# Performance work log

Hardware: AMD Instinct MI355X
Metric: run time of the kernel (lower is better)

## Reference

```python
import jax, jax.numpy as jnp
import numpy as np

EPS = 1e-5

def _instance_norm(x):
    # PyG InstanceNorm with batch=None, affine=False: per-channel normalize
    # over the node/edge dimension with biased variance.
    mean = jnp.mean(x, axis=0, keepdims=True)
    var = jnp.mean(jnp.square(x - mean), axis=0, keepdims=True)
    return (x - mean) * jax.lax.rsqrt(var + EPS)

def setup_inputs() -> dict:
    key = jax.random.key(0)
    ks = jax.random.split(key, 8)
    N, E, H = 50000, 800000, 64
    s1 = 1.0 / np.sqrt(2 * H)
    s2 = 1.0 / np.sqrt(4 * H)
    s3 = 1.0 / np.sqrt(H)
    return {
        "emb": jax.random.normal(ks[0], (N, H), dtype=jnp.float32),
        "edge_index": jax.random.randint(ks[1], (2, E), 0, N, dtype=jnp.int64),
        "W1": jax.random.normal(ks[2], (2 * H, 4 * H), dtype=jnp.float32) * s1,
        "b1": jnp.zeros((4 * H,), dtype=jnp.float32),
        "W2": jax.random.normal(ks[3], (4 * H, H), dtype=jnp.float32) * s2,
        "b2": jnp.zeros((H,), dtype=jnp.float32),
        "W3": jax.random.normal(ks[4], (H, 1), dtype=jnp.float32) * s3,
        "b3": jnp.zeros((1,), dtype=jnp.float32),
    }

def reference(emb, edge_index, W1, b1, W2, b2, W3, b3):
    # Dropout is identity in eval mode.
    col, row = edge_index[0], edge_index[1]
    f12 = jnp.concatenate([emb[col], emb[row]], axis=-1)  # [E, 2H]
    h = jax.nn.relu(_instance_norm(f12 @ W1 + b1))        # [E, 4H]
    h = jax.nn.relu(_instance_norm(h @ W2 + b2))          # [E, H]
    return h @ W3 + b3                                    # [E, 1]
```

## Files before the change

### kernel.cpp

```cpp
#include <hip/hip_runtime.h>
#include <stdint.h>

#define EPS 1e-5f

typedef __attribute__((ext_vector_type(8))) short bf16x8;
typedef __attribute__((ext_vector_type(4))) float f32x4;

__device__ __forceinline__ short f2bf(float f) {
  union { float f; unsigned u; } c; c.f = f;
  unsigned r = (c.u + 0x7FFFu + ((c.u >> 16) & 1u)) >> 16;
  return (short)r;
}
__device__ __forceinline__ float bf2f(unsigned short s) {
  union { unsigned u; float f; } c; c.u = ((unsigned)s) << 16;
  return c.f;
}

#define WS_SUM1 0
#define WS_SQ1  256
#define WS_SUM2 512
#define WS_SQ2  576
#define WS_M1   640
#define WS_I1   896
#define WS_M2   1152
#define WS_I2   1216
#define H2S_BYTE_OFF 8192

__global__ void k_zero(float* ws) {
  for (int i = threadIdx.x; i < 640; i += 256) ws[i] = 0.f;
}

__global__ void k_finalize(float* ws, int n, int so, int qo, int mo, int io, float invE) {
  int j = threadIdx.x;
  if (j < n) {
    float m = ws[so + j] * invE;
    float var = ws[qo + j] * invE - m * m;
    ws[mo + j] = m;
    ws[io + j] = rsqrtf(var + EPS);
  }
}

template <int MODE>
__global__ __launch_bounds__(256, 2) void fused_pass(
    const float* __restrict__ emb, const int* __restrict__ ei,
    const float* __restrict__ W1, const float* __restrict__ b1,
    const float* __restrict__ W2, const float* __restrict__ b2,
    const float* __restrict__ W3, const float* __restrict__ b3,
    float* __restrict__ ws, unsigned short* __restrict__ h2s,
    float* __restrict__ out, int E, int storeH2) {
  extern __shared__ __align__(16) char lds[];
  const int tid = threadIdx.x;
  const int lane = tid & 63;
  const int w = tid >> 6;
  const int l15 = lane & 15;
  const int l4 = lane >> 4;

  bf16x8 B1[4][4];
#pragma unroll
  for (int ni = 0; ni < 4; ++ni)
#pragma unroll
    for (int kk = 0; kk < 4; ++kk) {
      const int c = w * 64 + ni * 16 + l15;
      const int kb = kk * 32 + l4 * 8;
      bf16x8 v;
#pragma unroll
      for (int i = 0; i < 8; ++i) v[i] = f2bf(W1[(kb + i) * 256 + c]);
      B1[ni][kk] = v;
    }
  float b1v[4], m1v[4] = {0, 0, 0, 0}, i1v[4] = {0, 0, 0, 0};
#pragma unroll
  for (int ni = 0; ni < 4; ++ni) {
    const int c = w * 64 + ni * 16 + l15;
    b1v[ni] = b1[c];
    if (MODE >= 1) { m1v[ni] = ws[WS_M1 + c]; i1v[ni] = ws[WS_I1 + c]; }
  }
  bf16x8 B2[8];
  float b2v = 0.f, m2v = 0.f, i2v = 0.f, w3v = 0.f;
  if (MODE >= 1) {
#pragma unroll
    for (int kk = 0; kk < 8; ++kk) {
      const int c = w * 16 + l15;
      const int kb = kk * 32 + l4 * 8;
      bf16x8 v;
#pragma unroll
      for (int i = 0; i < 8; ++i) v[i] = f2bf(W2[(kb + i) * 64 + c]);
      B2[kk] = v;
    }
    b2v = b2[w * 16 + l15];
    if (MODE == 2) {
      m2v = ws[WS_M2 + w * 16 + l15];
      i2v = ws[WS_I2 + w * 16 + l15];
      w3v = W3[w * 16 + l15];
    }
  }

  float sAcc[4] = {0, 0, 0, 0}, qAcc[4] = {0, 0, 0, 0};
  float s2A = 0.f, q2A = 0.f;

  const int nTiles = E >> 6;
  for (int t = blockIdx.x; t < nTiles; t += gridDim.x) {
    const int e0 = t << 6;
    __syncthreads();

    {
      const int e = tid >> 2, q = tid & 3;
      const int nidx = (q < 2) ? ei[e0 + e] : ei[E + e0 + e];
      const float* src = emb + (long)nidx * 64 + (q & 1) * 32;
#pragma unroll
      for (int jj = 0; jj < 4; ++jj) {
        float4 fa = *reinterpret_cast<const float4*>(src + jj * 8);
        float4 fb = *reinterpret_cast<const float4*>(src + jj * 8 + 4);
        bf16x8 p;
        p[0] = f2bf(fa.x); p[1] = f2bf(fa.y); p[2] = f2bf(fa.z); p[3] = f2bf(fa.w);
        p[4] = f2bf(fb.x); p[5] = f2bf(fb.y); p[6] = f2bf(fb.z); p[7] = f2bf(fb.w);
        int byte = e * 256 + q * 64 + jj * 16;
        byte ^= (e & 7) << 4;
        *reinterpret_cast<bf16x8*>(lds + byte) = p;
      }
      if (MODE == 2) {
        if (tid < 64) reinterpret_cast<float*>(lds + 49152)[tid] = 0.f;
      }
    }
    __syncthreads();

    f32x4 acc[4][4];
#pragma unroll
    for (int mi = 0; mi < 4; ++mi)
#pragma unroll
      for (int ni = 0; ni < 4; ++ni) acc[mi][ni] = f32x4{0.f, 0.f, 0.f, 0.f};
#pragma unroll
    for (int kk = 0; kk < 4; ++kk) {
      bf16x8 af[4];
#pragma unroll
      for (int mi = 0; mi < 4; ++mi) {
        const int row = mi * 16 + l15;
        int byte = row * 256 + kk * 64 + l4 * 16;
        byte ^= (row & 7) << 4;
        af[mi] = *reinterpret_cast<const bf16x8*>(lds + byte);
      }
#pragma unroll
      for (int ni = 0; ni < 4; ++ni)
#pragma unroll
        for (int mi = 0; mi < 4; ++mi)
          acc[mi][ni] = __builtin_amdgcn_mfma_f32_16x16x32_bf16(af[mi], B1[ni][kk], acc[mi][ni], 0, 0, 0);
    }

    if (MODE == 0) {
#pragma unroll
      for (int mi = 0; mi < 4; ++mi)
#pragma unroll
        for (int ni = 0; ni < 4; ++ni)
#pragma unroll
          for (int r = 0; r < 4; ++r) {
            const float v = acc[mi][ni][r] + b1v[ni];
            sAcc[ni] += v;
            qAcc[ni] += v * v;
          }
    } else {
      char* g = lds + 16384;
#pragma unroll
      for (int mi = 0; mi < 4; ++mi)
#pragma unroll
        for (int ni = 0; ni < 4; ++ni) {
          const int c = w * 64 + ni * 16 + l15;
#pragma unroll
          for (int r = 0; r < 4; ++r) {
            const int row = mi * 16 + l4 * 4 + r;
            float v = (acc[mi][ni][r] + b1v[ni] - m1v[ni]) * i1v[ni];
            v = v > 0.f ? v : 0.f;
            int byte = row * 512 + c * 2;
            byte ^= (row & 7) << 4;
            *reinterpret_cast<short*>(g + byte) = f2bf(v);
          }
        }
      __syncthreads();

      f32x4 acc2[4];
#pragma unroll
      for (int mi = 0; mi < 4; ++mi) acc2[mi] = f32x4{0.f, 0.f, 0.f, 0.f};
#pragma unroll
      for (int kk = 0; kk < 8; ++kk) {
#pragma unroll
        for (int mi = 0; mi < 4; ++mi) {
          const int row = mi * 16 + l15;
          int byte = row * 512 + kk * 64 + l4 * 16;
          byte ^= (row & 7) << 4;
          const bf16x8 a2 = *reinterpret_cast<const bf16x8*>(g + byte);
          acc2[mi] = __builtin_amdgcn_mfma_f32_16x16x32_bf16(a2, B2[kk], acc2[mi], 0, 0, 0);
        }
      }

      if (MODE == 1) {
#pragma unroll
        for (int mi = 0; mi < 4; ++mi)
#pragma unroll
          for (int r = 0; r < 4; ++r) {
            const float v = acc2[mi][r] + b2v;
            s2A += v;
            q2A += v * v;
            if (storeH2) {
              const int row = e0 + mi * 16 + l4 * 4 + r;
              h2s[(size_t)row * 64 + w * 16 + l15] = (unsigned short)f2bf(v);
            }
          }
      } else {
        float* outp = reinterpret_cast<float*>(lds + 49152);
#pragma unroll
        for (int mi = 0; mi < 4; ++mi)
#pragma unroll
          for (int r = 0; r < 4; ++r) {
            const float v = acc2[mi][r] + b2v;
            float z = (v - m2v) * i2v;
            z = z > 0.f ? z : 0.f;
            float pv = z * w3v;
            pv += __shfl_xor(pv, 1);
            pv += __shfl_xor(pv, 2);
            pv += __shfl_xor(pv, 4);
            pv += __shfl_xor(pv, 8);
            if (l15 == 0) atomicAdd(&outp[mi * 16 + l4 * 4 + r], pv);
          }
        __syncthreads();
        if (tid < 64) out[e0 + tid] = outp[tid] + b3[0];
      }
    }
  }

  if (MODE == 0) {
#pragma unroll
    for (int ni = 0; ni < 4; ++ni) {
      float s = sAcc[ni], q = qAcc[ni];
      s += __shfl_xor(s, 16); s += __shfl_xor(s, 32);
      q += __shfl_xor(q, 16); q += __shfl_xor(q, 32);
      if (lane < 16) {
        atomicAdd(&ws[WS_SUM1 + w * 64 + ni * 16 + lane], s);
        atomicAdd(&ws[WS_SQ1 + w * 64 + ni * 16 + lane], q);
      }
    }
  }
  if (MODE == 1) {
    float s = s2A, q = q2A;
    s += __shfl_xor(s, 16); s += __shfl_xor(s, 32);
    q += __shfl_xor(q, 16); q += __shfl_xor(q, 32);
    if (lane < 16) {
      atomicAdd(&ws[WS_SUM2 + w * 16 + lane], s);
      atomicAdd(&ws[WS_SQ2 + w * 16 + lane], q);
    }
  }
}

__global__ void k_out(const unsigned short* __restrict__ h2s, const float* __restrict__ ws,
                      const float* __restrict__ W3, const float* __restrict__ b3,
                      float* __restrict__ out, int E) {
  __shared__ float sm[64], si[64], sw[64];
  const int tid = threadIdx.x;
  if (tid < 64) {
    sm[tid] = ws[WS_M2 + tid];
    si[tid] = ws[WS_I2 + tid];
    sw[tid] = W3[tid];
  }
  __syncthreads();
  const int e = blockIdx.x * 256 + tid;
  if (e >= E) return;
  const unsigned short* rp = h2s + (size_t)e * 64;
  float a = 0.f;
#pragma unroll
  for (int jj = 0; jj < 8; ++jj) {
    const bf16x8 v8 = *reinterpret_cast<const bf16x8*>(rp + jj * 8);
#pragma unroll
    for (int i = 0; i < 8; ++i) {
      const int j = jj * 8 + i;
      const float v = bf2f((unsigned short)v8[i]);
      float z = (v - sm[j]) * si[j];
      z = z > 0.f ? z : 0.f;
      a += z * sw[j];
    }
  }
  out[e] = a + b3[0];
}

extern "C" void kernel_launch(void* const* d_in, const int* in_sizes, int n_in,
                              void* d_out, int out_size, void* d_ws, size_t ws_size,
                              hipStream_t stream) {
  (void)n_in; (void)out_size;
  const float* emb = (const float*)d_in[0];
  const int* ei = (const int*)d_in[1];
  const float* W1 = (const float*)d_in[2];
  const float* b1 = (const float*)d_in[3];
  const float* W2 = (const float*)d_in[4];
  const float* b2 = (const float*)d_in[5];
  const float* W3 = (const float*)d_in[6];
  const float* b3 = (const float*)d_in[7];
  float* out = (float*)d_out;
  float* ws = (float*)d_ws;
  unsigned short* h2s = (unsigned short*)((char*)d_ws + H2S_BYTE_OFF);

  const int E = in_sizes[1] / 2;
  const int storeH2 = (ws_size >= (size_t)H2S_BYTE_OFF + (size_t)E * 64 * 2) ? 1 : 0;
  const float invE = 1.0f / (float)E;

  k_zero<<<1, 256, 0, stream>>>(ws);
  fused_pass<0><<<768, 256, 16384, stream>>>(emb, ei, W1, b1, W2, b2, W3, b3, ws, h2s, out, E, storeH2);
  k_finalize<<<1, 256, 0, stream>>>(ws, 256, WS_SUM1, WS_SQ1, WS_M1, WS_I1, invE);
  fused_pass<1><<<512, 256, 49152, stream>>>(emb, ei, W1, b1, W2, b2, W3, b3, ws, h2s, out, E, storeH2);
  k_finalize<<<1, 256, 0, stream>>>(ws, 64, WS_SUM2, WS_SQ2, WS_M2, WS_I2, invE);
  if (storeH2) {
    k_out<<<(E + 255) / 256, 256, 0, stream>>>(h2s, ws, W3, b3, out, E);
  } else {
    fused_pass<2><<<512, 256, 49152 + 256, stream>>>(emb, ei, W1, b1, W2, b2, W3, b3, ws, h2s, out, E, storeH2);
  }
}
```

Baseline: 845.4 us.

## Cache gathered bf16 edge features in workspace and reuse via async LDS loads

Pass 0 now writes the gathered, bf16-converted and swizzled [E,128] edge feature tiles to a workspace buffer, and pass 1 loads them straight into LDS with global_load_lds instead of redoing the random emb gather and conversion. The layer-2 staging buffer now reuses the same LDS region, with an extra barrier, which halves LDS per block. Launch bounds go to 4 blocks per CU and grids to 1024. The cost is an extra ~200MB of workspace writes and reads in exchange for avoiding a second random gather, and the path only runs if the workspace is large enough.

```diff
diff --git a/kernel.cpp b/kernel.cpp
--- a/kernel.cpp
+++ b/kernel.cpp
@@ -15,6 +15,11 @@
   union { unsigned u; float f; } c; c.u = ((unsigned)s) << 16;
   return c.f;
 }
+
+#define ASYNC_COPY16(gsrc, ldst)                                                   \
+  __builtin_amdgcn_global_load_lds(                                                \
+      (const __attribute__((address_space(1))) void*)(gsrc),                       \
+      (__attribute__((address_space(3))) void*)(ldst), 16, 0, 0)
 
 #define WS_SUM1 0
 #define WS_SQ1  256
@@ -40,14 +45,14 @@
   }
 }
 
-template <int MODE>
-__global__ __launch_bounds__(256, 2) void fused_pass(
+template <int MODE, int XT>
+__global__ __launch_bounds__(256, 4) void fused_pass(
     const float* __restrict__ emb, const int* __restrict__ ei,
     const float* __restrict__ W1, const float* __restrict__ b1,
     const float* __restrict__ W2, const float* __restrict__ b2,
     const float* __restrict__ W3, const float* __restrict__ b3,
     float* __restrict__ ws, unsigned short* __restrict__ h2s,
-    float* __restrict__ out, int E, int storeH2) {
+    char* __restrict__ f12s, float* __restrict__ out, int E, int storeH2) {
   extern __shared__ __align__(16) char lds[];
   const int tid = threadIdx.x;
   const int lane = tid & 63;
@@ -102,7 +107,13 @@
     const int e0 = t << 6;
     __syncthreads();
 
-    {
+    if (MODE == 1 && XT == 1) {
+      const char* src = f12s + (size_t)t * 16384 + w * 4096 + lane * 16;
+      char* dst = lds + w * 4096;
+#pragma unroll
+      for (int r = 0; r < 4; ++r)
+        ASYNC_COPY16(src + r * 1024, dst + r * 1024);
+    } else {
       const int e = tid >> 2, q = tid & 3;
       const int nidx = (q < 2) ? ei[e0 + e] : ei[E + e0 + e];
       const float* src = emb + (long)nidx * 64 + (q & 1) * 32;
@@ -117,11 +128,21 @@
         byte ^= (e & 7) << 4;
         *reinterpret_cast<bf16x8*>(lds + byte) = p;
       }
-      if (MODE == 2) {
-        if (tid < 64) reinterpret_cast<float*>(lds + 49152)[tid] = 0.f;
-      }
+    }
+    if (MODE == 2) {
+      if (tid < 64) reinterpret_cast<float*>(lds + 32768)[tid] = 0.f;
     }
     __syncthreads();
+
+    if (MODE == 0 && XT == 1) {
+      const char* srcL = lds + w * 4096;
+      char* dstG = f12s + (size_t)t * 16384 + w * 4096;
+#pragma unroll
+      for (int r = 0; r < 4; ++r) {
+        const bf16x8 v = *reinterpret_cast<const bf16x8*>(srcL + r * 1024 + lane * 16);
+        *reinterpret_cast<bf16x8*>(dstG + r * 1024 + lane * 16) = v;
+      }
+    }
 
     f32x4 acc[4][4];
 #pragma unroll
@@ -157,7 +178,9 @@
             qAcc[ni] += v * v;
           }
     } else {
-      char* g = lds + 16384;
+      __syncthreads();
+
+      char* g = lds;
 #pragma unroll
       for (int mi = 0; mi < 4; ++mi)
 #pragma unroll
@@ -204,7 +227,7 @@
             }
           }
       } else {
-        float* outp = reinterpret_cast<float*>(lds + 49152);
+        float* outp = reinterpret_cast<float*>(lds + 32768);
 #pragma unroll
         for (int mi = 0; mi < 4; ++mi)
 #pragma unroll
@@ -295,17 +318,26 @@
   unsigned short* h2s = (unsigned short*)((char*)d_ws + H2S_BYTE_OFF);
 
   const int E = in_sizes[1] / 2;
-  const int storeH2 = (ws_size >= (size_t)H2S_BYTE_OFF + (size_t)E * 64 * 2) ? 1 : 0;
+  const size_t h2bytes = (size_t)E * 64 * 2;
+  const size_t f12bytes = (size_t)E * 128 * 2;
+  char* f12s = (char*)d_ws + H2S_BYTE_OFF + h2bytes;
+  const int storeH2 = (ws_size >= (size_t)H2S_BYTE_OFF + h2bytes) ? 1 : 0;
+  const int storeF12 = (ws_size >= (size_t)H2S_BYTE_OFF + h2bytes + f12bytes) ? 1 : 0;
   const float invE = 1.0f / (float)E;
 
   k_zero<<<1, 256, 0, stream>>>(ws);
-  fused_pass<0><<<768, 256, 16384, stream>>>(emb, ei, W1, b1, W2, b2, W3, b3, ws, h2s, out, E, storeH2);
+  if (storeF12)
+    fused_pass<0, 1><<<1024, 256, 16384, stream>>>(emb, ei, W1, b1, W2, b2, W3, b3, ws, h2s, f12s, out, E, storeH2);
+  else
+    fused_pass<0, 0><<<1024, 256, 16384, stream>>>(emb, ei, W1, b1, W2, b2, W3, b3, ws, h2s, f12s, out, E, storeH2);
   k_finalize<<<1, 256, 0, stream>>>(ws, 256, WS_SUM1, WS_SQ1, WS_M1, WS_I1, invE);
-  fused_pass<1><<<512, 256, 49152, stream>>>(emb, ei, W1, b1, W2, b2, W3, b3, ws, h2s, out, E, storeH2);
+  if (storeF12)
+    fused_pass<1, 1><<<1024, 256, 32768, stream>>>(emb, ei, W1, b1, W2, b2, W3, b3, ws, h2s, f12s, out, E, storeH2);
+  else
+    fused_pass<1, 0><<<1024, 256, 32768, stream>>>(emb, ei, W1, b1, W2, b2, W3, b3, ws, h2s, f12s, out, E, storeH2);
   k_finalize<<<1, 256, 0, stream>>>(ws, 64, WS_SUM2, WS_SQ2, WS_M2, WS_I2, invE);
-  if (storeH2) {
+  if (storeH2)
     k_out<<<(E + 255) / 256, 256, 0, stream>>>(h2s, ws, W3, b3, out, E);
-  } else {
-    fused_pass<2><<<512, 256, 49152 + 256, stream>>>(emb, ei, W1, b1, W2, b2, W3, b3, ws, h2s, out, E, storeH2);
-  }
-}
+  else
+    fused_pass<2, 0><<<1024, 256, 33024, stream>>>(emb, ei, W1, b1, W2, b2, W3, b3, ws, h2s, f12s, out, E, storeH2);
+}
```

Measured after the change: 1.198 ms. 1.42x slower.

## Materialize bf16 layer-1 activations to avoid recomputing gather and first GEMM

Applied to the files above, without the earlier changes.

Adds a pass that gathers embeddings, computes the first GEMM once, accumulates its column statistics and writes the bf16 pre-norm activations to workspace as a swizzled LDS image. A second pass streams that image back with async global-to-LDS copies, applies norm and ReLU, and runs the second GEMM. This replaces the old scheme that recomputed the gather and first GEMM in the second pass. The cost is about 400MB of extra HBM traffic, and the path only runs when the workspace is large enough.

```diff
diff --git a/kernel.cpp b/kernel.cpp
--- a/kernel.cpp
+++ b/kernel.cpp
@@ -15,6 +15,11 @@
   union { unsigned u; float f; } c; c.u = ((unsigned)s) << 16;
   return c.f;
 }
+
+#define ASYNC_COPY16(gsrc, ldst)                                                   \
+  __builtin_amdgcn_global_load_lds(                                                \
+      (const __attribute__((address_space(1))) void*)(gsrc),                       \
+      (__attribute__((address_space(3))) void*)(ldst), 16, 0, 0)
 
 #define WS_SUM1 0
 #define WS_SQ1  256
@@ -37,6 +42,245 @@
     float var = ws[qo + j] * invE - m * m;
     ws[mo + j] = m;
     ws[io + j] = rsqrtf(var + EPS);
+  }
+}
+
+__global__ __launch_bounds__(256, 2) void k_pass_a(
+    const float* __restrict__ emb, const int* __restrict__ ei,
+    const float* __restrict__ W1, const float* __restrict__ b1,
+    float* __restrict__ ws, char* __restrict__ h1img, int E) {
+  extern __shared__ __align__(16) char lds[];
+  const int tid = threadIdx.x;
+  const int lane = tid & 63;
+  const int w = tid >> 6;
+  const int l15 = lane & 15;
+  const int l4 = lane >> 4;
+
+  bf16x8 B1[4][4];
+#pragma unroll
+  for (int ni = 0; ni < 4; ++ni)
+#pragma unroll
+    for (int kk = 0; kk < 4; ++kk) {
+      const int c = w * 64 + ni * 16 + l15;
+      const int kb = kk * 32 + l4 * 8;
+      bf16x8 v;
+#pragma unroll
+      for (int i = 0; i < 8; ++i) v[i] = f2bf(W1[(kb + i) * 256 + c]);
+      B1[ni][kk] = v;
+    }
+  float b1v[4];
+#pragma unroll
+  for (int ni = 0; ni < 4; ++ni) b1v[ni] = b1[w * 64 + ni * 16 + l15];
+
+  float sAcc[4] = {0, 0, 0, 0}, qAcc[4] = {0, 0, 0, 0};
+
+  const int nTiles = E >> 6;
+  const int e_ = tid >> 2, q_ = tid & 3;
+
+  float4 pf[8];
+  {
+    const int e0 = blockIdx.x << 6;
+    const int nidx = (q_ < 2) ? ei[e0 + e_] : ei[E + e0 + e_];
+    const float* src = emb + (long)nidx * 64 + (q_ & 1) * 32;
+#pragma unroll
+    for (int jj = 0; jj < 8; ++jj)
+      pf[jj] = *reinterpret_cast<const float4*>(src + jj * 4);
+  }
+
+  for (int t = blockIdx.x; t < nTiles; t += gridDim.x) {
+#pragma unroll
+    for (int jj = 0; jj < 4; ++jj) {
+      bf16x8 p;
+      p[0] = f2bf(pf[2 * jj].x); p[1] = f2bf(pf[2 * jj].y);
+      p[2] = f2bf(pf[2 * jj].z); p[3] = f2bf(pf[2 * jj].w);
+      p[4] = f2bf(pf[2 * jj + 1].x); p[5] = f2bf(pf[2 * jj + 1].y);
+      p[6] = f2bf(pf[2 * jj + 1].z); p[7] = f2bf(pf[2 * jj + 1].w);
+      int byte = e_ * 256 + q_ * 64 + jj * 16;
+      byte ^= (e_ & 7) << 4;
+      *reinterpret_cast<bf16x8*>(lds + byte) = p;
+    }
+    __syncthreads();
+
+    {
+      const int tn = t + (int)gridDim.x;
+      const int tv = (tn < nTiles) ? tn : t;
+      const int e0n = tv << 6;
+      const int nidx = (q_ < 2) ? ei[e0n + e_] : ei[E + e0n + e_];
+      const float* src = emb + (long)nidx * 64 + (q_ & 1) * 32;
+#pragma unroll
+      for (int jj = 0; jj < 8; ++jj)
+        pf[jj] = *reinterpret_cast<const float4*>(src + jj * 4);
+    }
+
+    f32x4 acc[4][4];
+#pragma unroll
+    for (int mi = 0; mi < 4; ++mi)
+#pragma unroll
+      for (int ni = 0; ni < 4; ++ni) acc[mi][ni] = f32x4{0.f, 0.f, 0.f, 0.f};
+#pragma unroll
+    for (int kk = 0; kk < 4; ++kk) {
+      bf16x8 af[4];
+#pragma unroll
+      for (int mi = 0; mi < 4; ++mi) {
+        const int row = mi * 16 + l15;
+        int byte = row * 256 + kk * 64 + l4 * 16;
+        byte ^= (row & 7) << 4;
+        af[mi] = *reinterpret_cast<const bf16x8*>(lds + byte);
+      }
+#pragma unroll
+      for (int ni = 0; ni < 4; ++ni)
+#pragma unroll
+        for (int mi = 0; mi < 4; ++mi)
+          acc[mi][ni] = __builtin_amdgcn_mfma_f32_16x16x32_bf16(af[mi], B1[ni][kk], acc[mi][ni], 0, 0, 0);
+    }
+
+    char* g = lds + 16384;
+#pragma unroll
+    for (int mi = 0; mi < 4; ++mi)
+#pragma unroll
+      for (int ni = 0; ni < 4; ++ni) {
+        const int c = w * 64 + ni * 16 + l15;
+#pragma unroll
+        for (int r = 0; r < 4; ++r) {
+          const int row = mi * 16 + l4 * 4 + r;
+          const short vb = f2bf(acc[mi][ni][r] + b1v[ni]);
+          const float vr = bf2f((unsigned short)vb);
+          sAcc[ni] += vr;
+          qAcc[ni] += vr * vr;
+          int byte = row * 512 + c * 2;
+          byte ^= (row & 7) << 4;
+          *reinterpret_cast<short*>(g + byte) = vb;
+        }
+      }
+    __syncthreads();
+
+    {
+      const char* srcL = lds + 16384 + w * 8192;
+      char* dstG = h1img + (size_t)t * 32768 + w * 8192;
+#pragma unroll
+      for (int r = 0; r < 8; ++r) {
+        const bf16x8 v = *reinterpret_cast<const bf16x8*>(srcL + r * 1024 + lane * 16);
+        __builtin_nontemporal_store(v, reinterpret_cast<bf16x8*>(dstG + r * 1024 + lane * 16));
+      }
+    }
+  }
+
+#pragma unroll
+  for (int ni = 0; ni < 4; ++ni) {
+    float s = sAcc[ni], q = qAcc[ni];
+    s += __shfl_xor(s, 16); s += __shfl_xor(s, 32);
+    q += __shfl_xor(q, 16); q += __shfl_xor(q, 32);
+    if (lane < 16) {
+      atomicAdd(&ws[WS_SUM1 + w * 64 + ni * 16 + lane], s);
+      atomicAdd(&ws[WS_SQ1 + w * 64 + ni * 16 + lane], q);
+    }
+  }
+}
+
+__global__ __launch_bounds__(256, 4) void k_pass_b(
+    const char* __restrict__ h1img, const float* __restrict__ W2,
+    const float* __restrict__ b2, float* __restrict__ ws,
+    unsigned short* __restrict__ h2s, int E) {
+  extern __shared__ __align__(16) char lds[];
+  const int tid = threadIdx.x;
+  const int lane = tid & 63;
+  const int w = tid >> 6;
+  const int l15 = lane & 15;
+  const int l4 = lane >> 4;
+
+  bf16x8 B2[8];
+#pragma unroll
+  for (int kk = 0; kk < 8; ++kk) {
+    const int c = w * 16 + l15;
+    const int kb = kk * 32 + l4 * 8;
+    bf16x8 v;
+#pragma unroll
+    for (int i = 0; i < 8; ++i) v[i] = f2bf(W2[(kb + i) * 64 + c]);
+    B2[kk] = v;
+  }
+  const float b2v = b2[w * 16 + l15];
+
+  reinterpret_cast<float*>(lds + 32768)[tid] = ws[WS_M1 + tid];
+  reinterpret_cast<float*>(lds + 33792)[tid] = ws[WS_I1 + tid];
+
+  float s2A = 0.f, q2A = 0.f;
+  const int nTiles = E >> 6;
+
+  for (int t = blockIdx.x; t < nTiles; t += gridDim.x) {
+    __syncthreads();
+
+    {
+      const char* src = h1img + (size_t)t * 32768 + w * 8192 + lane * 16;
+      char* dst = lds + w * 8192;
+#pragma unroll
+      for (int r = 0; r < 8; ++r)
+        ASYNC_COPY16(src + r * 1024, dst + r * 1024);
+    }
+    __syncthreads();
+
+    f32x4 acc2[4];
+#pragma unroll
+    for (int mi = 0; mi < 4; ++mi) acc2[mi] = f32x4{0.f, 0.f, 0.f, 0.f};
+#pragma unroll
+    for (int kk = 0; kk < 8; ++kk) {
+      const int cb = (kk * 32 + l4 * 8) * 4;
+      const float4 m1a = *reinterpret_cast<const float4*>(lds + 32768 + cb);
+      const float4 m1b = *reinterpret_cast<const float4*>(lds + 32768 + cb + 16);
+      const float4 i1a = *reinterpret_cast<const float4*>(lds + 33792 + cb);
+      const float4 i1b = *reinterpret_cast<const float4*>(lds + 33792 + cb + 16);
+      const float mv[8] = {m1a.x, m1a.y, m1a.z, m1a.w, m1b.x, m1b.y, m1b.z, m1b.w};
+      const float iv[8] = {i1a.x, i1a.y, i1a.z, i1a.w, i1b.x, i1b.y, i1b.z, i1b.w};
+#pragma unroll
+      for (int mi = 0; mi < 4; ++mi) {
+        const int row = mi * 16 + l15;
+        int byte = row * 512 + kk * 64 + l4 * 16;
+        byte ^= (row & 7) << 4;
+        const bf16x8 a = *reinterpret_cast<const bf16x8*>(lds + byte);
+        bf16x8 an;
+#pragma unroll
+        for (int i = 0; i < 8; ++i) {
+          float v = bf2f((unsigned short)a[i]);
+          v = (v - mv[i]) * iv[i];
+          an[i] = f2bf(v > 0.f ? v : 0.f);
+        }
+        acc2[mi] = __builtin_amdgcn_mfma_f32_16x16x32_bf16(an, B2[kk], acc2[mi], 0, 0, 0);
+      }
+    }
+    __syncthreads();
+
+#pragma unroll
+    for (int mi = 0; mi < 4; ++mi)
+#pragma unroll
+      for (int r = 0; r < 4; ++r) {
+        const int row = mi * 16 + l4 * 4 + r;
+        const float v = acc2[mi][r] + b2v;
+        s2A += v;
+        q2A += v * v;
+        int byte = row * 128 + (w * 16 + l15) * 2;
+        byte ^= ((row >> 2) & 3) << 5;
+        *reinterpret_cast<short*>(lds + byte) = f2bf(v);
+      }
+    __syncthreads();
+
+    {
+      const int row = tid >> 2, ch = tid & 3;
+      const int rb = row * 128 + ((ch * 32) ^ (((row >> 2) & 3) << 5));
+      const bf16x8 v0 = *reinterpret_cast<const bf16x8*>(lds + rb);
+      const bf16x8 v1 = *reinterpret_cast<const bf16x8*>(lds + rb + 16);
+      char* dstG = (char*)h2s + (size_t)t * 8192 + row * 128 + ch * 32;
+      __builtin_nontemporal_store(v0, reinterpret_cast<bf16x8*>(dstG));
+      __builtin_nontemporal_store(v1, reinterpret_cast<bf16x8*>(dstG + 16));
+    }
+  }
+
+  {
+    float s = s2A, q = q2A;
+    s += __shfl_xor(s, 16); s += __shfl_xor(s, 32);
+    q += __shfl_xor(q, 16); q += __shfl_xor(q, 32);
+    if (lane < 16) {
+      atomicAdd(&ws[WS_SUM2 + w * 16 + lane], s);
+      atomicAdd(&ws[WS_SQ2 + w * 16 + lane], q);
+    }
   }
 }
 
@@ -295,17 +539,28 @@
   unsigned short* h2s = (unsigned short*)((char*)d_ws + H2S_BYTE_OFF);
 
   const int E = in_sizes[1] / 2;
-  const int storeH2 = (ws_size >= (size_t)H2S_BYTE_OFF + (size_t)E * 64 * 2) ? 1 : 0;
+  const size_t h2bytes = (size_t)E * 64 * 2;
+  const size_t h1bytes = (size_t)E * 256 * 2;
+  char* h1img = (char*)d_ws + H2S_BYTE_OFF + h2bytes;
+  const int storeH2 = (ws_size >= (size_t)H2S_BYTE_OFF + h2bytes) ? 1 : 0;
+  const int storeH1 = (ws_size >= (size_t)H2S_BYTE_OFF + h2bytes + h1bytes) ? 1 : 0;
   const float invE = 1.0f / (float)E;
 
   k_zero<<<1, 256, 0, stream>>>(ws);
-  fused_pass<0><<<768, 256, 16384, stream>>>(emb, ei, W1, b1, W2, b2, W3, b3, ws, h2s, out, E, storeH2);
-  k_finalize<<<1, 256, 0, stream>>>(ws, 256, WS_SUM1, WS_SQ1, WS_M1, WS_I1, invE);
-  fused_pass<1><<<512, 256, 49152, stream>>>(emb, ei, W1, b1, W2, b2, W3, b3, ws, h2s, out, E, storeH2);
-  k_finalize<<<1, 256, 0, stream>>>(ws, 64, WS_SUM2, WS_SQ2, WS_M2, WS_I2, invE);
-  if (storeH2) {
+  if (storeH1) {
+    k_pass_a<<<1024, 256, 49152, stream>>>(emb, ei, W1, b1, ws, h1img, E);
+    k_finalize<<<1, 256, 0, stream>>>(ws, 256, WS_SUM1, WS_SQ1, WS_M1, WS_I1, invE);
+    k_pass_b<<<2048, 256, 34816, stream>>>(h1img, W2, b2, ws, h2s, E);
+    k_finalize<<<1, 256, 0, stream>>>(ws, 64, WS_SUM2, WS_SQ2, WS_M2, WS_I2, invE);
     k_out<<<(E + 255) / 256, 256, 0, stream>>>(h2s, ws, W3, b3, out, E);
   } else {
-    fused_pass<2><<<512, 256, 49152 + 256, stream>>>(emb, ei, W1, b1, W2, b2, W3, b3, ws, h2s, out, E, storeH2);
-  }
-}
+    fused_pass<0><<<768, 256, 16384, stream>>>(emb, ei, W1, b1, W2, b2, W3, b3, ws, h2s, out, E, storeH2);
+    k_finalize<<<1, 256, 0, stream>>>(ws, 256, WS_SUM1, WS_SQ1, WS_M1, WS_I1, invE);
+    fused_pass<1><<<512, 256, 49152, stream>>>(emb, ei, W1, b1, W2, b2, W3, b3, ws, h2s, out, E, storeH2);
+    k_finalize<<<1, 256, 0, stream>>>(ws, 64, WS_SUM2, WS_SQ2, WS_M2, WS_I2, invE);
+    if (storeH2)
+      k_out<<<(E + 255) / 256, 256, 0, stream>>>(h2s, ws, W3, b3, out, E);
+    else
+      fused_pass<2><<<512, 256, 49408, stream>>>(emb, ei, W1, b1, W2, b2, W3, b3, ws, h2s, out, E, storeH2);
+  }
+}
```

Result: no change. 844.0 us (-0.2%).
